# Performance work log

Measured on AMD Instinct MI355X. Metric: run time of the kernel, lower is better.

## Reference

```python
import jax, jax.numpy as jnp
import numpy as np
from jax import lax

BS, Q, T, D, NC = 64, 1024, 128, 2, 20
COST_CLASS = 1.0
COST_BBOX = 1.0
INF = jnp.float32(1e30)


def setup_inputs() -> dict:
    key = jax.random.key(0)
    k1, k2, k3, k4 = jax.random.split(key, 4)
    pred_logits = jax.random.normal(k1, (BS, Q, NC), dtype=jnp.float32)
    pred_coords = jax.random.uniform(k2, (BS, Q, D), dtype=jnp.float32)
    tgt_labels = jax.random.randint(k3, (BS, T), 0, NC, dtype=jnp.int32)
    tgt_joints = jax.random.uniform(k4, (BS, T, D), dtype=jnp.float32)
    return {"pred_logits": pred_logits, "pred_coords": pred_coords,
            "tgt_labels": tgt_labels, "tgt_joints": tgt_joints}


def cost_matrix(pred_logits, pred_coords, tgt_labels, tgt_joints):
    # C[b, q, t] = cost_bbox * L1(coords) + cost_class * (-softmax(logits)[label_t])
    B, Qn, _ = pred_logits.shape
    Tn = tgt_labels.shape[1]
    out_prob = jax.nn.softmax(pred_logits, axis=-1)                     # (B,Q,NC)
    idx = jnp.broadcast_to(tgt_labels[:, None, :], (B, Qn, Tn))         # (B,Q,T)
    cost_class = -jnp.take_along_axis(out_prob, idx, axis=2)           # (B,Q,T)
    cost_bbox = jnp.sum(jnp.abs(pred_coords[:, :, None, :]
                                - tgt_joints[:, None, :, :]), axis=-1)  # (B,Q,T)
    return COST_BBOX * cost_bbox + COST_CLASS * cost_class


def _lsa(cost):
    """Rectangular linear sum assignment (shortest augmenting path / JV),
    cost: (n, m) with n <= m. Returns col4row: assigned column per row."""
    n, m = cost.shape
    rows = jnp.arange(n, dtype=jnp.int32)

    def solve_row(state, cur_row):
        u, v, col4row, row4col = state

        def sp_cond(s):
            return s[0] < 0

        def sp_body(s):
            sink, i, minVal, SC, spc, path = s
            r = minVal + cost[i] - u[i] - v                     # (m,) reduced costs
            upd = (~SC) & (r < spc)
            spc = jnp.where(upd, r, spc)
            path = jnp.where(upd, i, path)
            masked = jnp.where(SC, INF, spc)
            j = jnp.argmin(masked).astype(jnp.int32)
            minVal = masked[j]
            SC = SC.at[j].set(True)
            sink = jnp.where(row4col[j] < 0, j, jnp.int32(-1))
            i = row4col[j]
            return sink, i, minVal, SC, spc, path

        init = (jnp.int32(-1), cur_row, jnp.float32(0.0),
                jnp.zeros((m,), bool), jnp.full((m,), INF),
                jnp.zeros((m,), jnp.int32))
        sink, _, minVal, SC, spc, path = lax.while_loop(sp_cond, sp_body, init)

        # dual updates (as in scipy's implementation)
        u = u.at[cur_row].add(minVal)
        assigned = (col4row >= 0) & (rows != cur_row)
        on_path = assigned & (path[jnp.clip(col4row, 0)] >= 0)  # rows scanned (SR)
        # rows in SR other than cur_row: those whose assigned col got relaxed & is in SC
        sr_other = assigned & SC[jnp.clip(col4row, 0)]
        u = u + jnp.where(sr_other, minVal - spc[jnp.clip(col4row, 0)], 0.0)
        v = v - jnp.where(SC, minVal - spc, 0.0)

        # augment along alternating path ending at sink
        def aug_cond(s):
            return ~s[3]

        def aug_body(s):
            j, c4r, r4c, done = s
            i = path[j]
            r4c = r4c.at[j].set(i)
            nj = c4r[i]
            c4r = c4r.at[i].set(j)
            return nj, c4r, r4c, (i == cur_row)

        _, col4row, row4col, _ = lax.while_loop(
            aug_cond, aug_body, (sink, col4row, row4col, jnp.bool_(False)))
        return (u, v, col4row, row4col), None

    init_state = (jnp.zeros((n,), jnp.float32), jnp.zeros((m,), jnp.float32),
                  jnp.full((n,), -1, jnp.int32), jnp.full((m,), -1, jnp.int32))
    (_, _, col4row, _), _ = lax.scan(solve_row, init_state, rows)
    return col4row


def reference(pred_logits, pred_coords, tgt_labels, tgt_joints):
    C = cost_matrix(pred_logits, pred_coords, tgt_labels, tgt_joints)  # (B,Q,T)
    # Q > T, so (like scipy) solve on the transpose: rows = targets, cols = queries
    col4row = jax.vmap(_lsa)(jnp.transpose(C, (0, 2, 1)))              # (B,T) query per target
    order = jnp.argsort(col4row, axis=-1).astype(jnp.int32)            # sort by pred index
    pred_idx = jnp.take_along_axis(col4row, order, axis=-1)            # (B,T)
    tgt_idx = order                                                    # (B,T)
    return pred_idx, tgt_idx
```

## Files before the change

### kernel.cpp

```cpp
#include <hip/hip_runtime.h>

#define BSZ 64
#define QN  1024
#define TN  128
#define NCL 20
#define INFV 1e30f

typedef float f32x2 __attribute__((ext_vector_type(2)));
typedef float f32x4 __attribute__((ext_vector_type(4)));

template<int CTRL>
__device__ __forceinline__ float dpp_min(float x) {
    int r = __builtin_amdgcn_mov_dpp(__float_as_int(x), CTRL, 0xF, 0xF, false);
    return fminf(x, __int_as_float(r));
}
__device__ __forceinline__ float min3f(float a, float b, float c) {
    float d;
    asm("v_min3_f32 %0, %1, %2, %3" : "=v"(d) : "v"(a), "v"(b), "v"(c));
    return d;
}
__device__ __forceinline__ float swap32_min(float x) {
    float a = x, b = x;
    asm volatile("v_permlane32_swap_b32 %0, %1" : "+v"(a), "+v"(b));
    return min3f(x, a, b);
}
__device__ __forceinline__ float swap16_min(float x) {
    float a = x, b = x;
    asm volatile("v_permlane16_swap_b32 %0, %1" : "+v"(a), "+v"(b));
    return min3f(x, a, b);
}
__device__ __forceinline__ int rdl(int v, int l) {
    return __builtin_amdgcn_readlane(v, l);
}
__device__ __forceinline__ float rdlf(float v, int l) {
    return __int_as_float(__builtin_amdgcn_readlane(__float_as_int(v), l));
}

__global__ __launch_bounds__(256) void lsa_fused_kernel(
    const float* __restrict__ pred_logits,
    const float* __restrict__ pred_coords,
    const int*   __restrict__ tgt_labels,
    const float* __restrict__ tgt_joints,
    int*         __restrict__ out)
{
    const int b    = blockIdx.x;
    const int tid  = threadIdx.x;
    const int w    = tid >> 6;
    const int lane = tid & 63;

    __shared__ __align__(16) float    probP[NCL * QN];
    __shared__ __align__(16) float    cmS[QN];
    __shared__ uint32_t pthBW[QN / 4];
    __shared__ uint8_t  labsB[TN];
    __shared__ int      c4rS[TN];
    __shared__ __align__(16) int comm[16];

    {
        const float* lg = pred_logits + (size_t)b * QN * NCL;
#pragma unroll
        for (int k = 0; k < 4; ++k) {
            int q = tid * 4 + k;
            const f32x4* rp = (const f32x4*)(lg + (size_t)q * NCL);
            float x[NCL];
            *(f32x4*)&x[0]  = rp[0];
            *(f32x4*)&x[4]  = rp[1];
            *(f32x4*)&x[8]  = rp[2];
            *(f32x4*)&x[12] = rp[3];
            *(f32x4*)&x[16] = rp[4];
            float mx = x[0];
#pragma unroll
            for (int c = 1; c < NCL; ++c) mx = fmaxf(mx, x[c]);
            float e[NCL];
            float ssum = 0.f;
#pragma unroll
            for (int c = 0; c < NCL; ++c) { e[c] = expf(x[c] - mx); ssum += e[c]; }
#pragma unroll
            for (int c = 0; c < NCL; ++c) probP[c * QN + q] = e[c] / ssum;
        }
    }
    if (tid < TN) labsB[tid] = (uint8_t)(tgt_labels[(size_t)b * TN + tid] & 0xFF);

    const int c0 = w * 256 + lane * 4;
    const float2* pcg = (const float2*)pred_coords + (size_t)b * QN;
    f32x2 pxp[2], pyp[2], vvp[2];
#pragma unroll
    for (int s = 0; s < 4; ++s) {
        float2 P = pcg[c0 + s];
        pxp[s >> 1][s & 1] = P.x;
        pyp[s >> 1][s & 1] = P.y;
        vvp[s >> 1][s & 1] = 0.f;
    }
    int rc[4];
    int pk[4];
#pragma unroll
    for (int s = 0; s < 4; ++s) { rc[s] = 0xFF; pk[s] = (c0 + s) | (0xFF << 10); }

    const int*    labsg = tgt_labels + (size_t)b * TN;
    const float2* tjg   = (const float2*)tgt_joints + (size_t)b * TN;
    int    labAB = (labsg[lane] & 0xFF) | ((labsg[lane + 64] & 0xFF) << 8);
    float2 tjA = tjg[lane], tjB = tjg[lane + 64];
    float  u0 = 0.f, u1 = 0.f;
    int    c4rA = -1, c4rB = -1;
    __syncthreads();

    int par = 0;
    f32x4 pr4;
    float tx, ty, u_i;
    {
        int labI = rdl(labAB, 0) & 0xFF;
        pr4 = *(const f32x4*)&probP[labI * QN + c0];
        tx = rdlf(tjA.x, 0); ty = rdlf(tjA.y, 0); u_i = rdlf(u0, 0);
    }

    for (int cur = 0; cur < TN; ++cur) {
        float sp[4];
        int   pth[4];
        unsigned scMask = 0;
#pragma unroll
        for (int s = 0; s < 4; ++s) { sp[s] = INFV; pth[s] = 0; }

        float minVal = 0.f;
        int   i_s = cur, sinkJ = -1, iters = 0;

        while (true) {
            f32x2 tx2 = {tx, tx}, ty2 = {ty, ty};
            f32x2 mv2 = {minVal, minVal}, ui2 = {u_i, u_i};
            float mval[4];
#pragma unroll
            for (int p = 0; p < 2; ++p) {
                f32x2 pr; pr[0] = pr4[p * 2]; pr[1] = pr4[p * 2 + 1];
                f32x2 dx = pxp[p] - tx2;
                f32x2 dy = pyp[p] - ty2;
                f32x2 cb = __builtin_elementwise_abs(dx) + __builtin_elementwise_abs(dy);
                f32x2 cost = cb - pr;
                f32x2 r2 = ((mv2 + cost) - ui2) - vvp[p];
#pragma unroll
                for (int e = 0; e < 2; ++e) {
                    const int s = p * 2 + e;
                    bool unm = ((scMask >> s) & 1u) == 0u;
                    float r = r2[e];
                    bool upd = unm && (r < sp[s]);
                    sp[s]   = upd ? r   : sp[s];
                    pth[s]  = upd ? i_s : pth[s];
                    mval[s] = unm ? sp[s] : INFV;
                }
            }
            bool t1 = mval[1] < mval[0];
            float vA = t1 ? mval[1] : mval[0]; int kA = t1 ? pk[1] : pk[0];
            bool t2 = mval[3] < mval[2];
            float vB = t2 ? mval[3] : mval[2]; int kB = t2 ? pk[3] : pk[2];
            bool t3 = vB < vA;
            float lmin = t3 ? vB : vA;  int lpk = t3 ? kB : kA;

            float g = swap32_min(lmin);
            g = swap16_min(g);
            g = dpp_min<0x128>(g); g = dpp_min<0x124>(g);
            g = dpp_min<0x122>(g); g = dpp_min<0x121>(g);
            float gw = __int_as_float(
                __builtin_amdgcn_readfirstlane(__float_as_int(g)));
            unsigned long long mk = __ballot(lmin == gw);
            int L = __ffsll(mk) - 1;
            int wpk = rdl(lpk, L);

            if (lane == 0)
                *(int2*)&comm[par * 8 + w * 2] = make_int2(__float_as_int(gw), wpk);
            __syncthreads();
            int4 ra = *(const int4*)&comm[par * 8 + 0];
            int4 rb = *(const int4*)&comm[par * 8 + 4];
            par ^= 1;
            float v0 = __int_as_float(ra.x), v1 = __int_as_float(ra.z);
            float v2 = __int_as_float(rb.x), v3 = __int_as_float(rb.z);
            bool s1 = v1 < v0; float vX = s1 ? v1 : v0; int kX = s1 ? ra.w : ra.y;
            bool s2 = v3 < v2; float vY = s2 ? v3 : v2; int kY = s2 ? rb.w : rb.y;
            bool s3 = vY < vX; float gv = s3 ? vY : vX; int gpk = s3 ? kY : kX;
            minVal = gv;

            const int j     = gpk & 1023;
            const int rbyte = (gpk >> 10) & 0xFF;
            sinkJ = j;
            if (w == (j >> 8) && lane == ((j >> 2) & 63))
                scMask |= 1u << (j & 3);
            if (rbyte == 0xFF) break;
            if (++iters > QN + 2) break;

            const int labI = gpk >> 18;
            pr4 = *(const f32x4*)&probP[labI * QN + c0];
            i_s = rbyte;
            bool hi = i_s >= 64; int l6 = i_s & 63;
            tx  = rdlf(hi ? tjB.x : tjA.x, l6);
            ty  = rdlf(hi ? tjB.y : tjA.y, l6);
            u_i = rdlf(hi ? u1 : u0, l6);
        }

        f32x4 dmp;
#pragma unroll
        for (int s = 0; s < 4; ++s)
            dmp[s] = ((scMask >> s) & 1u) ? sp[s] : INFV;
        *(f32x4*)&cmS[c0] = dmp;
        pthBW[(unsigned)c0 >> 2] =
            (uint32_t)(pth[0] & 0xFF)        | ((uint32_t)(pth[1] & 0xFF) << 8) |
            ((uint32_t)(pth[2] & 0xFF) << 16) | ((uint32_t)(pth[3] & 0xFF) << 24);
        const int c4A_old = c4rA, c4B_old = c4rB;
        __syncthreads();

        float wvA = cmS[c4A_old < 0 ? 0 : c4A_old];
        float wvB = cmS[c4B_old < 0 ? 0 : c4B_old];

        {
            const uint8_t* pthB = (const uint8_t*)pthBW;
            int jx = sinkJ;
            for (int it = 0; it <= TN; ++it) {
                int ii = pthB[jx];
                bool me = (w == (jx >> 8)) && (lane == ((jx >> 2) & 63));
                int sl = jx & 3;
#pragma unroll
                for (int s = 0; s < 4; ++s)
                    rc[s] = (me && s == sl) ? ii : rc[s];
                bool hi2 = ii >= 64; int cown = ii & 63;
                int nj = rdl(hi2 ? c4rB : c4rA, cown);
                if (lane == cown) { if (hi2) c4rB = jx; else c4rA = jx; }
                jx = nj;
                if (ii == cur) break;
            }
        }

#pragma unroll
        for (int s = 0; s < 4; ++s) {
            if ((scMask >> s) & 1u)
                vvp[s >> 1][s & 1] -= (minVal - sp[s]);
        }
#pragma unroll
        for (int s = 0; s < 4; ++s) {
            int lr = labsB[rc[s] & 127];
            pk[s] = (c0 + s) | (rc[s] << 10) | (lr << 18);
        }

        if (lane == (cur & 63)) {
            if (cur >= 64) u1 += minVal; else u0 += minVal;
        }
        if (lane != cur && c4A_old >= 0 && wvA < 5e29f) u0 += minVal - wvA;
        {
            int rr = lane + 64;
            if (rr != cur && c4B_old >= 0 && wvB < 5e29f) u1 += minVal - wvB;
        }

        {
            int curN = (cur < TN - 1) ? cur + 1 : TN - 1;
            int lw = rdl(labAB, curN & 63);
            int labI = (lw >> ((curN >> 6) * 8)) & 0xFF;
            pr4 = *(const f32x4*)&probP[labI * QN + c0];
            bool hi = curN >= 64; int l6 = curN & 63;
            tx  = rdlf(hi ? tjB.x : tjA.x, l6);
            ty  = rdlf(hi ? tjB.y : tjA.y, l6);
            u_i = rdlf(hi ? u1 : u0, l6);
        }
    }

    if (w == 0) { c4rS[lane] = c4rA; c4rS[lane + 64] = c4rB; }
    __syncthreads();
    if (tid < TN) {
        int t = tid;
        int q = c4rS[t];
        int rank = 0;
        for (int s = 0; s < TN; ++s) rank += (c4rS[s] < q) ? 1 : 0;
        out[(size_t)b * TN + rank] = q;
        out[(size_t)(BSZ + b) * TN + rank] = t;
    }
}

extern "C" void kernel_launch(void* const* d_in, const int* in_sizes, int n_in,
                              void* d_out, int out_size, void* d_ws, size_t ws_size,
                              hipStream_t stream) {
    const float* pred_logits = (const float*)d_in[0];
    const float* pred_coords = (const float*)d_in[1];
    const int*   tgt_labels  = (const int*)d_in[2];
    const float* tgt_joints  = (const float*)d_in[3];

    lsa_fused_kernel<<<BSZ, 256, 0, stream>>>(pred_logits, pred_coords,
                                              tgt_labels, tgt_joints,
                                              (int*)d_out);
}
```

Measured before the change: 176.0 us.

## Replace per-iteration block barrier with tagged LDS mailbox spin-wait

The cross-wave argmin exchange inside the shortest-path loop no longer uses __syncthreads. Each wave now writes a 64-bit packed (value, key, sequence tag) word into a double-buffered LDS mailbox and spins until all four slots carry the current tag. This removes a full workgroup barrier from the innermost serial loop. The cost is busy-wait polling on volatile LDS, a reliance on ordering between waves that no fence enforces, and an 8-bit tag that has to stay unambiguous across the two buffers.

```diff
diff --git a/kernel.cpp b/kernel.cpp
--- a/kernel.cpp
+++ b/kernel.cpp
@@ -53,7 +53,7 @@
     __shared__ uint32_t pthBW[QN / 4];
     __shared__ uint8_t  labsB[TN];
     __shared__ int      c4rS[TN];
-    __shared__ __align__(16) int comm[16];
+    __shared__ __align__(16) unsigned long long commLL[8];
 
     {
         const float* lg = pred_logits + (size_t)b * QN * NCL;
@@ -79,6 +79,7 @@
         }
     }
     if (tid < TN) labsB[tid] = (uint8_t)(tgt_labels[(size_t)b * TN + tid] & 0xFF);
+    if (tid < 8)  commLL[tid] = 0ull;
 
     const int c0 = w * 256 + lane * 4;
     const float2* pcg = (const float2*)pred_coords + (size_t)b * QN;
@@ -103,7 +104,7 @@
     int    c4rA = -1, c4rB = -1;
     __syncthreads();
 
-    int par = 0;
+    unsigned gseq = 1;
     f32x4 pr4;
     float tx, ty, u_i;
     {
@@ -162,17 +163,37 @@
             int L = __ffsll(mk) - 1;
             int wpk = rdl(lpk, L);
 
-            if (lane == 0)
-                *(int2*)&comm[par * 8 + w * 2] = make_int2(__float_as_int(gw), wpk);
-            __syncthreads();
-            int4 ra = *(const int4*)&comm[par * 8 + 0];
-            int4 rb = *(const int4*)&comm[par * 8 + 4];
-            par ^= 1;
-            float v0 = __int_as_float(ra.x), v1 = __int_as_float(ra.z);
-            float v2 = __int_as_float(rb.x), v3 = __int_as_float(rb.z);
-            bool s1 = v1 < v0; float vX = s1 ? v1 : v0; int kX = s1 ? ra.w : ra.y;
-            bool s2 = v3 < v2; float vY = s2 ? v3 : v2; int kY = s2 ? rb.w : rb.y;
-            bool s3 = vY < vX; float gv = s3 ? vY : vX; int gpk = s3 ? kY : kX;
+            const unsigned tag = gseq & 0xFFu;
+            volatile unsigned long long* mb =
+                (volatile unsigned long long*)&commLL[(gseq & 1u) * 4];
+            {
+                unsigned hi = (unsigned)wpk | (tag << 24);
+                unsigned long long pack =
+                    ((unsigned long long)hi << 32) | (unsigned)__float_as_int(gw);
+                if (lane == 0) mb[w] = pack;
+            }
+            unsigned long long s0, s1, s2, s3;
+            int guardp = 0;
+            for (;;) {
+                s0 = mb[0]; s1 = mb[1]; s2 = mb[2]; s3 = mb[3];
+                bool ok = ((unsigned)(s0 >> 56) == tag) &
+                          ((unsigned)(s1 >> 56) == tag) &
+                          ((unsigned)(s2 >> 56) == tag) &
+                          ((unsigned)(s3 >> 56) == tag);
+                if (ok) break;
+                if (++guardp > (1 << 18)) break;
+            }
+            ++gseq;
+
+            float v0 = __int_as_float((int)(unsigned)s0);
+            float v1 = __int_as_float((int)(unsigned)s1);
+            float v2 = __int_as_float((int)(unsigned)s2);
+            float v3 = __int_as_float((int)(unsigned)s3);
+            int k0 = (int)(unsigned)(s0 >> 32), k1 = (int)(unsigned)(s1 >> 32);
+            int k2 = (int)(unsigned)(s2 >> 32), k3 = (int)(unsigned)(s3 >> 32);
+            bool b1 = v1 < v0; float vX = b1 ? v1 : v0; int kX = b1 ? k1 : k0;
+            bool b2 = v3 < v2; float vY = b2 ? v3 : v2; int kY = b2 ? k3 : k2;
+            bool b3 = vY < vX; float gv = b3 ? vY : vX; int gpk = b3 ? kY : kX;
             minVal = gv;
 
             const int j     = gpk & 1023;
@@ -183,7 +204,7 @@
             if (rbyte == 0xFF) break;
             if (++iters > QN + 2) break;
 
-            const int labI = gpk >> 18;
+            const int labI = (gpk >> 18) & 0x1F;
             pr4 = *(const f32x4*)&probP[labI * QN + c0];
             i_s = rbyte;
             bool hi = i_s >= 64; int l6 = i_s & 63;
```

Result: slower. 198.2 us (+12.6%).
